# Optimization experiments

Measured on AMD Instinct MI355X. Metric: run time of the kernel, lower is better.

Reference implementation:

```python
import jax, jax.numpy as jnp
import numpy as np

N_NODES = 50000
N_EDGES = 1600000
D = 64


def setup_inputs() -> dict:
    key = jax.random.key(0)
    ks = jax.random.split(key, 7)
    scale = 1.0 / np.sqrt(2 * D)  # keep activations sane through relu stack
    x = jax.random.normal(ks[0], (N_NODES, D), dtype=jnp.float32)
    edge_index = jax.random.randint(ks[1], (2, N_EDGES), 0, N_NODES, dtype=jnp.int32)
    edge_weight = jax.random.uniform(ks[2], (N_EDGES,), dtype=jnp.float32)
    W1 = jax.random.normal(ks[3], (D, 2 * D), dtype=jnp.float32) * scale
    b1 = jax.random.normal(ks[4], (D,), dtype=jnp.float32) * 0.01
    W2 = jax.random.normal(ks[5], (D, 2 * D), dtype=jnp.float32) * scale
    b2 = jax.random.normal(ks[6], (D,), dtype=jnp.float32) * 0.01
    return {"x": x, "edge_index": edge_index, "edge_weight": edge_weight,
            "W1": W1, "b1": b1, "W2": W2, "b2": b2}


def _sage_conv(x, src, dst, edge_weight, W, b):
    # gather neighbor features, weight, scatter-mean onto src nodes
    m = x[dst] * edge_weight[:, None]                      # [E, d]
    agg_sum = jax.ops.segment_sum(m, src, num_segments=x.shape[0])
    cnt = jax.ops.segment_sum(jnp.ones_like(edge_weight), src,
                              num_segments=x.shape[0])
    agg = agg_sum / jnp.maximum(cnt, 1.0)[:, None]          # scatter 'mean'
    h = jnp.concatenate([x, agg], axis=1)                   # [N, 2d]
    return h @ W.T + b


def reference(x, edge_index, edge_weight, W1, b1, W2, b2):
    src, dst = edge_index[0], edge_index[1]
    h = jax.nn.relu(_sage_conv(x, src, dst, edge_weight, W1, b1))
    h = jax.nn.relu(_sage_conv(h, src, dst, edge_weight, W2, b2))
    return h
```

## Files before the change

### kernel.cpp

```cpp
#include <hip/hip_runtime.h>

#define NN 50000
#define NE 1600000
#define DD 64
#define NPB 196
#define HPB 98
#define NBKT 256
#define CHUNK 2500
#define NBLK 640
#define SLOT 24
#define SSTR 25
#define S1CAP 1024
#define SPCAP 512
#define ELLW 80

typedef __attribute__((ext_vector_type(8))) short bf16x8;
typedef __attribute__((ext_vector_type(4))) float f32x4;
typedef __attribute__((ext_vector_type(2))) float f32x2;

static __device__ __forceinline__ unsigned short f2bf(float f) {
    unsigned int u = __float_as_uint(f);
    unsigned int r = (u + 0x7FFFu + ((u >> 16) & 1u)) >> 16;
    return (unsigned short)r;
}
static __device__ __forceinline__ float bf2f(unsigned short h) {
    return __uint_as_float((unsigned int)h << 16);
}
static __device__ __forceinline__ unsigned int pk_fp8x4(float a, float b, float c, float d) {
    unsigned int p = __builtin_amdgcn_cvt_pk_fp8_f32(a, b, 0u, false);
    p = __builtin_amdgcn_cvt_pk_fp8_f32(c, d, p, true);
    return p;
}

__global__ __launch_bounds__(256) void prep_bin(
    const int* __restrict__ ei, const float* __restrict__ ew,
    int* __restrict__ gcur, int* __restrict__ gspillc,
    int2* __restrict__ buf1, int2* __restrict__ spill,
    const float* __restrict__ x, ushort* __restrict__ xb,
    unsigned int* __restrict__ xf8,
    const float* __restrict__ W1, const float* __restrict__ W2,
    ushort* __restrict__ W1b, ushort* __restrict__ W2b)
{
    __shared__ int2 slot[NBKT * SSTR];
    __shared__ int  lcnt[NBKT];
    __shared__ int  lbase[NBKT];
    int tid = threadIdx.x;
    int blk = blockIdx.x;

    if (blk >= NBLK) {
        int pb = blk - NBLK;
        if (pb < 3125) {
            int i = pb * 256 + tid;
            float4 v = ((const float4*)x)[i];
            ushort4 o;
            o.x = f2bf(v.x); o.y = f2bf(v.y); o.z = f2bf(v.z); o.w = f2bf(v.w);
            ((ushort4*)xb)[i] = o;
            xf8[i] = pk_fp8x4(v.x, v.y, v.z, v.w);
        } else {
            int i = (pb - 3125) * 256 + tid;
            const float* src = (i < 2048) ? W1 : W2;
            ushort* dst = (i < 2048) ? W1b : W2b;
            int j = i & 2047;
            float4 v = ((const float4*)src)[j];
            ushort4 o;
            o.x = f2bf(v.x); o.y = f2bf(v.y); o.z = f2bf(v.z); o.w = f2bf(v.w);
            ((ushort4*)dst)[j] = o;
        }
        return;
    }

    int shard = blk & 7;
    for (int b = tid; b < NBKT; b += 256) lcnt[b] = 0;
    __syncthreads();

    int g0 = blk * (CHUNK / 4);
    const int4*   s4 = (const int4*)ei;
    const int4*   d4 = ((const int4*)ei) + NE / 4;
    const float4* w4 = (const float4*)ew;
    for (int it = 0; it < 3; ++it) {
        int idx = it * 256 + tid;
        if (idx >= CHUNK / 4) break;
        int4 sv = s4[g0 + idx];
        int4 dv = d4[g0 + idx];
        float4 wv = w4[g0 + idx];
#pragma unroll
        for (int k = 0; k < 4; ++k) {
            int s = (k == 0) ? sv.x : (k == 1) ? sv.y : (k == 2) ? sv.z : sv.w;
            int d = (k == 0) ? dv.x : (k == 1) ? dv.y : (k == 2) ? dv.z : dv.w;
            float w = (k == 0) ? wv.x : (k == 1) ? wv.y : (k == 2) ? wv.z : wv.w;
            int bkt = s / NPB;
            int sloc = s - bkt * NPB;
            int2 rec = make_int2(d | ((int)f2bf(w) << 16), sloc);
            int pos = atomicAdd(&lcnt[bkt], 1);
            if (pos < SLOT) {
                slot[bkt * SSTR + pos] = rec;
            } else {
                int sp = atomicAdd(&gspillc[bkt], 1);
                if (sp < SPCAP) spill[bkt * SPCAP + sp] = rec;
            }
        }
    }
    __syncthreads();

    {
        int b = tid;
        int n = lcnt[b]; if (n > SLOT) n = SLOT;
        lcnt[b] = n;
        lbase[b] = (n > 0) ? atomicAdd(&gcur[b * 8 + shard], n) : 0;
    }
    __syncthreads();

    int wave = tid >> 6, lane = tid & 63;
    int grp = lane >> 4, l16 = lane & 15;
#pragma unroll 4
    for (int jj = 0; jj < 16; ++jj) {
        int b = wave * 64 + jj * 4 + grp;
        int n = lcnt[b];
        int base = lbase[b];
        int2* dst = &buf1[((size_t)b * 8 + shard) * S1CAP];
        if (l16 < n) {
            int2 rec = slot[b * SSTR + l16];
            int p = base + l16;
            if (p < S1CAP) dst[p] = rec;
            else { int sp = atomicAdd(&gspillc[b], 1);
                   if (sp < SPCAP) spill[b * SPCAP + sp] = rec; }
        }
        if (l16 + 16 < n) {
            int2 rec = slot[b * SSTR + l16 + 16];
            int p = base + l16 + 16;
            if (p < S1CAP) dst[p] = rec;
            else { int sp = atomicAdd(&gspillc[b], 1);
                   if (sp < SPCAP) spill[b * SPCAP + sp] = rec; }
        }
    }
}

__global__ __launch_bounds__(1024) void build_ell(
    const int* __restrict__ gcur, const int2* __restrict__ buf1,
    const int* __restrict__ gspillc, const int2* __restrict__ spill,
    unsigned int* __restrict__ csr, int* __restrict__ cnt)
{
    __shared__ int cur[HPB];
    __shared__ int cnts[9];
    int tid = threadIdx.x;
    int bkt  = blockIdx.x >> 1;
    int nlo  = (blockIdx.x & 1) * HPB;

    if (tid < HPB) cur[tid] = 0;
    if (tid >= 128 && tid < 137) {
        int sh = tid - 128;
        int n = (sh < 8) ? gcur[bkt * 8 + sh] : gspillc[bkt];
        int cap = (sh < 8) ? S1CAP : SPCAP;
        cnts[sh] = n < cap ? n : cap;
    }
    __syncthreads();

    {
        int sh = tid >> 7, lt = tid & 127;
        int n = cnts[sh];
        const int2* rp = buf1 + ((size_t)bkt * 8 + sh) * S1CAP;
        for (int i = lt; i < n; i += 128) {
            int2 r = rp[i];
            int node = r.y - nlo;
            if ((unsigned)node < HPB) {
                int pos = atomicAdd(&cur[node], 1);
                if (pos < ELLW)
                    csr[((size_t)(bkt * NPB + r.y)) * ELLW + pos] = (unsigned int)r.x;
            }
        }
    }
    {
        int n = cnts[8];
        const int2* rp = spill + (size_t)bkt * SPCAP;
        for (int i = tid; i < n; i += 1024) {
            int2 r = rp[i];
            int node = r.y - nlo;
            if ((unsigned)node < HPB) {
                int pos = atomicAdd(&cur[node], 1);
                if (pos < ELLW)
                    csr[((size_t)(bkt * NPB + r.y)) * ELLW + pos] = (unsigned int)r.x;
            }
        }
    }
    __syncthreads();

    if (tid < HPB) {
        int node = bkt * NPB + nlo + tid;
        if (node < NN) {
            int deg = cur[tid];
            cnt[node] = deg;
            int c = deg < ELLW ? deg : ELLW;
            int c16 = (c + 15) & ~15;
            for (int p = c; p < c16; ++p)
                csr[(size_t)node * ELLW + p] = 0u;
        }
    }
}

#define PROC16(r, s01, s23)                                                   \
    {                                                                         \
        unsigned int v0 = f8[(r.x & 0xFFFF) * 16 + l16];                      \
        unsigned int v1 = f8[(r.y & 0xFFFF) * 16 + l16];                      \
        unsigned int v2 = f8[(r.z & 0xFFFF) * 16 + l16];                      \
        unsigned int v3 = f8[(r.w & 0xFFFF) * 16 + l16];                      \
        float w0 = __uint_as_float(r.x & 0xFFFF0000u);                        \
        float w1 = __uint_as_float(r.y & 0xFFFF0000u);                        \
        float w2 = __uint_as_float(r.z & 0xFFFF0000u);                        \
        float w3 = __uint_as_float(r.w & 0xFFFF0000u);                        \
        f32x2 lo, hi, wp;                                                     \
        lo = __builtin_amdgcn_cvt_pk_f32_fp8(v0, false);                      \
        hi = __builtin_amdgcn_cvt_pk_f32_fp8(v0, true);                       \
        wp = (f32x2){w0, w0}; s01 += wp * lo; s23 += wp * hi;                 \
        lo = __builtin_amdgcn_cvt_pk_f32_fp8(v1, false);                      \
        hi = __builtin_amdgcn_cvt_pk_f32_fp8(v1, true);                       \
        wp = (f32x2){w1, w1}; s01 += wp * lo; s23 += wp * hi;                 \
        lo = __builtin_amdgcn_cvt_pk_f32_fp8(v2, false);                      \
        hi = __builtin_amdgcn_cvt_pk_f32_fp8(v2, true);                       \
        wp = (f32x2){w2, w2}; s01 += wp * lo; s23 += wp * hi;                 \
        lo = __builtin_amdgcn_cvt_pk_f32_fp8(v3, false);                      \
        hi = __builtin_amdgcn_cvt_pk_f32_fp8(v3, true);                       \
        wp = (f32x2){w3, w3}; s01 += wp * lo; s23 += wp * hi;                 \
    }

__global__ __launch_bounds__(512) void fused_layer(
    const ushort* __restrict__ Xb,
    const unsigned int* __restrict__ f8,
    const int* __restrict__ cnt, const unsigned int* __restrict__ csr,
    const ushort* __restrict__ Wb, const float* __restrict__ bias,
    float* __restrict__ out, ushort* __restrict__ outb,
    unsigned char* __restrict__ outf8)
{
    __shared__ ushort xL[16][72];
    __shared__ ushort aggL[16][72];
    int tid = threadIdx.x;
    int wave = tid >> 6, lane = tid & 63;
    int g = lane >> 4, l16 = lane & 15;
    int base = blockIdx.x * 16;
    int nodeA = base + wave;
    int nodeB = base + wave + 8;

    if (lane < 16) {
        *(ushort4*)&xL[wave][l16 * 4] =
            *(const ushort4*)&Xb[(size_t)nodeA * DD + l16 * 4];
        *(ushort4*)&xL[wave + 8][l16 * 4] =
            *(const ushort4*)&Xb[(size_t)nodeB * DD + l16 * 4];
    }

    int ndA = cnt[nodeA], ndB = cnt[nodeB];
    int nA = ndA < ELLW ? ndA : ELLW;
    int nB = ndB < ELLW ? ndB : ELLW;
    int nA16 = (nA + 15) & ~15;
    int nB16 = (nB + 15) & ~15;
    int imax = nA16 > nB16 ? nA16 : nB16;
    const unsigned int* __restrict__ rpA = csr + (size_t)nodeA * ELLW + g * 4;
    const unsigned int* __restrict__ rpB = csr + (size_t)nodeB * ELLW + g * 4;
    f32x2 sA01 = {0.f, 0.f}, sA23 = {0.f, 0.f};
    f32x2 sB01 = {0.f, 0.f}, sB23 = {0.f, 0.f};

    uint4 rA, rB;
    if (0 < nA16) rA = *(const uint4*)(rpA);
    if (0 < nB16) rB = *(const uint4*)(rpB);

    for (int i = 0; i < imax; i += 16) {
        uint4 rAn, rBn;
        bool doAn = (i + 16) < nA16, doBn = (i + 16) < nB16;
        if (doAn) rAn = *(const uint4*)(rpA + i + 16);
        if (doBn) rBn = *(const uint4*)(rpB + i + 16);
        bool doA = i < nA16, doB = i < nB16;
        if (doA) PROC16(rA, sA01, sA23);
        if (doB) PROC16(rB, sB01, sB23);
        rA = rAn; rB = rBn;
    }

    float aA0 = sA01.x, aA1 = sA01.y, aA2 = sA23.x, aA3 = sA23.y;
    float aB0 = sB01.x, aB1 = sB01.y, aB2 = sB23.x, aB3 = sB23.y;
    aA0 += __shfl_xor(aA0, 16); aA0 += __shfl_xor(aA0, 32);
    aA1 += __shfl_xor(aA1, 16); aA1 += __shfl_xor(aA1, 32);
    aA2 += __shfl_xor(aA2, 16); aA2 += __shfl_xor(aA2, 32);
    aA3 += __shfl_xor(aA3, 16); aA3 += __shfl_xor(aA3, 32);
    aB0 += __shfl_xor(aB0, 16); aB0 += __shfl_xor(aB0, 32);
    aB1 += __shfl_xor(aB1, 16); aB1 += __shfl_xor(aB1, 32);
    aB2 += __shfl_xor(aB2, 16); aB2 += __shfl_xor(aB2, 32);
    aB3 += __shfl_xor(aB3, 16); aB3 += __shfl_xor(aB3, 32);

    if (lane < 16) {
        float dmA = (float)(ndA > 1 ? ndA : 1);
        float dmB = (float)(ndB > 1 ? ndB : 1);
        ushort4 oA, oB;
        oA.x = f2bf(aA0 / dmA); oA.y = f2bf(aA1 / dmA);
        oA.z = f2bf(aA2 / dmA); oA.w = f2bf(aA3 / dmA);
        oB.x = f2bf(aB0 / dmB); oB.y = f2bf(aB1 / dmB);
        oB.z = f2bf(aB2 / dmB); oB.w = f2bf(aB3 / dmB);
        *(ushort4*)&aggL[wave][l16 * 4] = oA;
        *(ushort4*)&aggL[wave + 8][l16 * 4] = oB;
    }
    __syncthreads();

    if (wave < 4) {
        f32x4 acc = (f32x4){0.f, 0.f, 0.f, 0.f};
#pragma unroll
        for (int ki = 0; ki < 4; ++ki) {
            const ushort* ap = (ki < 2) ? &xL[l16][ki * 32 + g * 8]
                                        : &aggL[l16][(ki - 2) * 32 + g * 8];
            bf16x8 af = *(const bf16x8*)ap;
            bf16x8 bfrag = *(const bf16x8*)&Wb[(size_t)(wave * 16 + l16) * 128 + ki * 32 + g * 8];
            acc = __builtin_amdgcn_mfma_f32_16x16x32_bf16(af, bfrag, acc, 0, 0, 0);
        }
        int col = wave * 16 + l16;
        float bv = bias[col];
#pragma unroll
        for (int r = 0; r < 4; ++r) {
            int grow = base + g * 4 + r;
            float v = fmaxf(acc[r] + bv, 0.f);
            if (out)  out[(size_t)grow * DD + col] = v;
            if (outb) outb[(size_t)grow * DD + col] = f2bf(v);
            if (outf8) {
                unsigned int p = __builtin_amdgcn_cvt_pk_fp8_f32(v, v, 0u, false);
                outf8[(size_t)grow * DD + col] = (unsigned char)(p & 0xFFu);
            }
        }
    }
}

extern "C" void kernel_launch(void* const* d_in, const int* in_sizes, int n_in,
                              void* d_out, int out_size, void* d_ws, size_t ws_size,
                              hipStream_t stream)
{
    const float* x  = (const float*)d_in[0];
    const int*   ei = (const int*)d_in[1];
    const float* ew = (const float*)d_in[2];
    const float* W1 = (const float*)d_in[3];
    const float* b1 = (const float*)d_in[4];
    const float* W2 = (const float*)d_in[5];
    const float* b2 = (const float*)d_in[6];
    float* out = (float*)d_out;

    char* ws = (char*)d_ws;
    int*          gcur    = (int*)ws;
    int*          gspillc = (int*)(ws + 8192);
    int2*         buf1    = (int2*)(ws + 16384);
    int2*         spill   = (int2*)(ws + 16793600);
    unsigned int* csr     = (unsigned int*)(ws + 17842176);
    int*          cnt     = (int*)(ws + 33898496);
    ushort*       xb      = (ushort*)(ws + 34099200);
    ushort*       h1b     = (ushort*)(ws + 40499200);
    ushort*       W1b     = (ushort*)(ws + 46899200);
    ushort*       W2b     = (ushort*)(ws + 46915584);
    unsigned int* xf8     = (unsigned int*)(ws + 46931968);
    unsigned char* h1f8   = (unsigned char*)(ws + 50131968);

    hipMemsetAsync(gcur, 0, 9216, stream);

    prep_bin<<<NBLK + 3141, 256, 0, stream>>>(ei, ew, gcur, gspillc, buf1, spill,
                                              x, xb, xf8, W1, W2, W1b, W2b);
    build_ell<<<NBKT * 2, 1024, 0, stream>>>(gcur, buf1, gspillc, spill, csr, cnt);

    fused_layer<<<NN / 16, 512, 0, stream>>>(xb, xf8, cnt, csr, W1b, b1,
                                             nullptr, h1b, h1f8);
    fused_layer<<<NN / 16, 512, 0, stream>>>(h1b, (const unsigned int*)h1f8,
                                             cnt, csr, W2b, b2, out, nullptr, nullptr);
}
```

Measured before the change: 172.4 us.

## Merge all stages into one persistent kernel with software grid barriers

Replaces the four kernel launches (binning, ELL build, two fused SAGE layers) with a single persistent kernel of 512 blocks of 1024 threads. The stages are separated by atomic-counter grid barriers, and shared memory is reused through a union. This removes launch gaps and tail effects between stages. In exchange, the grid barriers add spin cost, occupancy during the layers is fixed, and correctness relies on all 512 blocks being co-resident.

```diff
diff --git a/kernel.cpp b/kernel.cpp
--- a/kernel.cpp
+++ b/kernel.cpp
@@ -6,13 +6,15 @@
 #define NPB 196
 #define HPB 98
 #define NBKT 256
-#define CHUNK 2500
-#define NBLK 640
+#define NCHUNK 640
+#define CG 625
 #define SLOT 24
 #define SSTR 25
 #define S1CAP 1024
 #define SPCAP 512
 #define ELLW 80
+#define GRID 512
+#define NTILE 1563
 
 typedef __attribute__((ext_vector_type(8))) short bf16x8;
 typedef __attribute__((ext_vector_type(4))) float f32x4;
@@ -23,178 +25,31 @@
     unsigned int r = (u + 0x7FFFu + ((u >> 16) & 1u)) >> 16;
     return (unsigned short)r;
 }
-static __device__ __forceinline__ float bf2f(unsigned short h) {
-    return __uint_as_float((unsigned int)h << 16);
-}
 static __device__ __forceinline__ unsigned int pk_fp8x4(float a, float b, float c, float d) {
     unsigned int p = __builtin_amdgcn_cvt_pk_fp8_f32(a, b, 0u, false);
     p = __builtin_amdgcn_cvt_pk_fp8_f32(c, d, p, true);
     return p;
 }
 
-__global__ __launch_bounds__(256) void prep_bin(
-    const int* __restrict__ ei, const float* __restrict__ ew,
-    int* __restrict__ gcur, int* __restrict__ gspillc,
-    int2* __restrict__ buf1, int2* __restrict__ spill,
-    const float* __restrict__ x, ushort* __restrict__ xb,
-    unsigned int* __restrict__ xf8,
-    const float* __restrict__ W1, const float* __restrict__ W2,
-    ushort* __restrict__ W1b, ushort* __restrict__ W2b)
-{
-    __shared__ int2 slot[NBKT * SSTR];
-    __shared__ int  lcnt[NBKT];
-    __shared__ int  lbase[NBKT];
-    int tid = threadIdx.x;
-    int blk = blockIdx.x;
-
-    if (blk >= NBLK) {
-        int pb = blk - NBLK;
-        if (pb < 3125) {
-            int i = pb * 256 + tid;
-            float4 v = ((const float4*)x)[i];
-            ushort4 o;
-            o.x = f2bf(v.x); o.y = f2bf(v.y); o.z = f2bf(v.z); o.w = f2bf(v.w);
-            ((ushort4*)xb)[i] = o;
-            xf8[i] = pk_fp8x4(v.x, v.y, v.z, v.w);
+static __device__ __forceinline__ void gridbar(int* bar) {
+    __syncthreads();
+    if (threadIdx.x == 0) {
+        int my = __hip_atomic_load(&bar[1], __ATOMIC_RELAXED, __HIP_MEMORY_SCOPE_AGENT);
+        __threadfence();
+        if (atomicAdd(&bar[0], 1) == GRID - 1) {
+            bar[0] = 0;
+            __threadfence();
+            __hip_atomic_store(&bar[1], my + 1, __ATOMIC_RELEASE, __HIP_MEMORY_SCOPE_AGENT);
         } else {
-            int i = (pb - 3125) * 256 + tid;
-            const float* src = (i < 2048) ? W1 : W2;
-            ushort* dst = (i < 2048) ? W1b : W2b;
-            int j = i & 2047;
-            float4 v = ((const float4*)src)[j];
-            ushort4 o;
-            o.x = f2bf(v.x); o.y = f2bf(v.y); o.z = f2bf(v.z); o.w = f2bf(v.w);
-            ((ushort4*)dst)[j] = o;
-        }
-        return;
-    }
-
-    int shard = blk & 7;
-    for (int b = tid; b < NBKT; b += 256) lcnt[b] = 0;
+            int t = 0;
+            while (__hip_atomic_load(&bar[1], __ATOMIC_ACQUIRE, __HIP_MEMORY_SCOPE_AGENT) == my) {
+                __builtin_amdgcn_s_sleep(4);
+                if (++t > (1 << 22)) break;
+            }
+        }
+        __threadfence();
+    }
     __syncthreads();
-
-    int g0 = blk * (CHUNK / 4);
-    const int4*   s4 = (const int4*)ei;
-    const int4*   d4 = ((const int4*)ei) + NE / 4;
-    const float4* w4 = (const float4*)ew;
-    for (int it = 0; it < 3; ++it) {
-        int idx = it * 256 + tid;
-        if (idx >= CHUNK / 4) break;
-        int4 sv = s4[g0 + idx];
-        int4 dv = d4[g0 + idx];
-        float4 wv = w4[g0 + idx];
-#pragma unroll
-        for (int k = 0; k < 4; ++k) {
-            int s = (k == 0) ? sv.x : (k == 1) ? sv.y : (k == 2) ? sv.z : sv.w;
-            int d = (k == 0) ? dv.x : (k == 1) ? dv.y : (k == 2) ? dv.z : dv.w;
-            float w = (k == 0) ? wv.x : (k == 1) ? wv.y : (k == 2) ? wv.z : wv.w;
-            int bkt = s / NPB;
-            int sloc = s - bkt * NPB;
-            int2 rec = make_int2(d | ((int)f2bf(w) << 16), sloc);
-            int pos = atomicAdd(&lcnt[bkt], 1);
-            if (pos < SLOT) {
-                slot[bkt * SSTR + pos] = rec;
-            } else {
-                int sp = atomicAdd(&gspillc[bkt], 1);
-                if (sp < SPCAP) spill[bkt * SPCAP + sp] = rec;
-            }
-        }
-    }
-    __syncthreads();
-
-    {
-        int b = tid;
-        int n = lcnt[b]; if (n > SLOT) n = SLOT;
-        lcnt[b] = n;
-        lbase[b] = (n > 0) ? atomicAdd(&gcur[b * 8 + shard], n) : 0;
-    }
-    __syncthreads();
-
-    int wave = tid >> 6, lane = tid & 63;
-    int grp = lane >> 4, l16 = lane & 15;
-#pragma unroll 4
-    for (int jj = 0; jj < 16; ++jj) {
-        int b = wave * 64 + jj * 4 + grp;
-        int n = lcnt[b];
-        int base = lbase[b];
-        int2* dst = &buf1[((size_t)b * 8 + shard) * S1CAP];
-        if (l16 < n) {
-            int2 rec = slot[b * SSTR + l16];
-            int p = base + l16;
-            if (p < S1CAP) dst[p] = rec;
-            else { int sp = atomicAdd(&gspillc[b], 1);
-                   if (sp < SPCAP) spill[b * SPCAP + sp] = rec; }
-        }
-        if (l16 + 16 < n) {
-            int2 rec = slot[b * SSTR + l16 + 16];
-            int p = base + l16 + 16;
-            if (p < S1CAP) dst[p] = rec;
-            else { int sp = atomicAdd(&gspillc[b], 1);
-                   if (sp < SPCAP) spill[b * SPCAP + sp] = rec; }
-        }
-    }
-}
-
-__global__ __launch_bounds__(1024) void build_ell(
-    const int* __restrict__ gcur, const int2* __restrict__ buf1,
-    const int* __restrict__ gspillc, const int2* __restrict__ spill,
-    unsigned int* __restrict__ csr, int* __restrict__ cnt)
-{
-    __shared__ int cur[HPB];
-    __shared__ int cnts[9];
-    int tid = threadIdx.x;
-    int bkt  = blockIdx.x >> 1;
-    int nlo  = (blockIdx.x & 1) * HPB;
-
-    if (tid < HPB) cur[tid] = 0;
-    if (tid >= 128 && tid < 137) {
-        int sh = tid - 128;
-        int n = (sh < 8) ? gcur[bkt * 8 + sh] : gspillc[bkt];
-        int cap = (sh < 8) ? S1CAP : SPCAP;
-        cnts[sh] = n < cap ? n : cap;
-    }
-    __syncthreads();
-
-    {
-        int sh = tid >> 7, lt = tid & 127;
-        int n = cnts[sh];
-        const int2* rp = buf1 + ((size_t)bkt * 8 + sh) * S1CAP;
-        for (int i = lt; i < n; i += 128) {
-            int2 r = rp[i];
-            int node = r.y - nlo;
-            if ((unsigned)node < HPB) {
-                int pos = atomicAdd(&cur[node], 1);
-                if (pos < ELLW)
-                    csr[((size_t)(bkt * NPB + r.y)) * ELLW + pos] = (unsigned int)r.x;
-            }
-        }
-    }
-    {
-        int n = cnts[8];
-        const int2* rp = spill + (size_t)bkt * SPCAP;
-        for (int i = tid; i < n; i += 1024) {
-            int2 r = rp[i];
-            int node = r.y - nlo;
-            if ((unsigned)node < HPB) {
-                int pos = atomicAdd(&cur[node], 1);
-                if (pos < ELLW)
-                    csr[((size_t)(bkt * NPB + r.y)) * ELLW + pos] = (unsigned int)r.x;
-            }
-        }
-    }
-    __syncthreads();
-
-    if (tid < HPB) {
-        int node = bkt * NPB + nlo + tid;
-        if (node < NN) {
-            int deg = cur[tid];
-            cnt[node] = deg;
-            int c = deg < ELLW ? deg : ELLW;
-            int c16 = (c + 15) & ~15;
-            for (int p = c; p < c16; ++p)
-                csr[(size_t)node * ELLW + p] = 0u;
-        }
-    }
 }
 
 #define PROC16(r, s01, s23)                                                   \
@@ -222,104 +77,285 @@
         wp = (f32x2){w3, w3}; s01 += wp * lo; s23 += wp * hi;                 \
     }
 
-__global__ __launch_bounds__(512) void fused_layer(
-    const ushort* __restrict__ Xb,
-    const unsigned int* __restrict__ f8,
+static __device__ void fused_phase(
+    const ushort* __restrict__ Xb, const unsigned int* __restrict__ f8,
     const int* __restrict__ cnt, const unsigned int* __restrict__ csr,
     const ushort* __restrict__ Wb, const float* __restrict__ bias,
     float* __restrict__ out, ushort* __restrict__ outb,
-    unsigned char* __restrict__ outf8)
+    unsigned char* __restrict__ outf8,
+    ushort (*xL)[72], ushort (*aggL)[72])
 {
-    __shared__ ushort xL[16][72];
-    __shared__ ushort aggL[16][72];
     int tid = threadIdx.x;
     int wave = tid >> 6, lane = tid & 63;
+    int sub = wave >> 3, w8 = wave & 7;
     int g = lane >> 4, l16 = lane & 15;
-    int base = blockIdx.x * 16;
-    int nodeA = base + wave;
-    int nodeB = base + wave + 8;
-
-    if (lane < 16) {
-        *(ushort4*)&xL[wave][l16 * 4] =
-            *(const ushort4*)&Xb[(size_t)nodeA * DD + l16 * 4];
-        *(ushort4*)&xL[wave + 8][l16 * 4] =
-            *(const ushort4*)&Xb[(size_t)nodeB * DD + l16 * 4];
-    }
-
-    int ndA = cnt[nodeA], ndB = cnt[nodeB];
-    int nA = ndA < ELLW ? ndA : ELLW;
-    int nB = ndB < ELLW ? ndB : ELLW;
-    int nA16 = (nA + 15) & ~15;
-    int nB16 = (nB + 15) & ~15;
-    int imax = nA16 > nB16 ? nA16 : nB16;
-    const unsigned int* __restrict__ rpA = csr + (size_t)nodeA * ELLW + g * 4;
-    const unsigned int* __restrict__ rpB = csr + (size_t)nodeB * ELLW + g * 4;
-    f32x2 sA01 = {0.f, 0.f}, sA23 = {0.f, 0.f};
-    f32x2 sB01 = {0.f, 0.f}, sB23 = {0.f, 0.f};
-
-    uint4 rA, rB;
-    if (0 < nA16) rA = *(const uint4*)(rpA);
-    if (0 < nB16) rB = *(const uint4*)(rpB);
-
-    for (int i = 0; i < imax; i += 16) {
-        uint4 rAn, rBn;
-        bool doAn = (i + 16) < nA16, doBn = (i + 16) < nB16;
-        if (doAn) rAn = *(const uint4*)(rpA + i + 16);
-        if (doBn) rBn = *(const uint4*)(rpB + i + 16);
-        bool doA = i < nA16, doB = i < nB16;
-        if (doA) PROC16(rA, sA01, sA23);
-        if (doB) PROC16(rB, sB01, sB23);
-        rA = rAn; rB = rBn;
-    }
-
-    float aA0 = sA01.x, aA1 = sA01.y, aA2 = sA23.x, aA3 = sA23.y;
-    float aB0 = sB01.x, aB1 = sB01.y, aB2 = sB23.x, aB3 = sB23.y;
-    aA0 += __shfl_xor(aA0, 16); aA0 += __shfl_xor(aA0, 32);
-    aA1 += __shfl_xor(aA1, 16); aA1 += __shfl_xor(aA1, 32);
-    aA2 += __shfl_xor(aA2, 16); aA2 += __shfl_xor(aA2, 32);
-    aA3 += __shfl_xor(aA3, 16); aA3 += __shfl_xor(aA3, 32);
-    aB0 += __shfl_xor(aB0, 16); aB0 += __shfl_xor(aB0, 32);
-    aB1 += __shfl_xor(aB1, 16); aB1 += __shfl_xor(aB1, 32);
-    aB2 += __shfl_xor(aB2, 16); aB2 += __shfl_xor(aB2, 32);
-    aB3 += __shfl_xor(aB3, 16); aB3 += __shfl_xor(aB3, 32);
-
-    if (lane < 16) {
-        float dmA = (float)(ndA > 1 ? ndA : 1);
-        float dmB = (float)(ndB > 1 ? ndB : 1);
-        ushort4 oA, oB;
-        oA.x = f2bf(aA0 / dmA); oA.y = f2bf(aA1 / dmA);
-        oA.z = f2bf(aA2 / dmA); oA.w = f2bf(aA3 / dmA);
-        oB.x = f2bf(aB0 / dmB); oB.y = f2bf(aB1 / dmB);
-        oB.z = f2bf(aB2 / dmB); oB.w = f2bf(aB3 / dmB);
-        *(ushort4*)&aggL[wave][l16 * 4] = oA;
-        *(ushort4*)&aggL[wave + 8][l16 * 4] = oB;
-    }
-    __syncthreads();
-
-    if (wave < 4) {
-        f32x4 acc = (f32x4){0.f, 0.f, 0.f, 0.f};
+
+    for (int t = blockIdx.x; t < NTILE; t += GRID) {
+        int base16 = t * 32 + sub * 16;
+        int nodeA = base16 + w8;
+        int nodeB = base16 + w8 + 8;
+        bool vA = nodeA < NN, vB = nodeB < NN;
+        int rowA = sub * 16 + w8, rowB = rowA + 8;
+
+        if (lane < 16) {
+            ushort4 z = make_ushort4(0, 0, 0, 0);
+            *(ushort4*)&xL[rowA][l16 * 4] = vA
+                ? *(const ushort4*)&Xb[(size_t)nodeA * DD + l16 * 4] : z;
+            *(ushort4*)&xL[rowB][l16 * 4] = vB
+                ? *(const ushort4*)&Xb[(size_t)nodeB * DD + l16 * 4] : z;
+        }
+
+        int ndA = vA ? cnt[nodeA] : 0;
+        int ndB = vB ? cnt[nodeB] : 0;
+        int nA = ndA < ELLW ? ndA : ELLW;
+        int nB = ndB < ELLW ? ndB : ELLW;
+        int nA16 = (nA + 15) & ~15;
+        int nB16 = (nB + 15) & ~15;
+        int imax = nA16 > nB16 ? nA16 : nB16;
+        const unsigned int* rpA = csr + (size_t)(vA ? nodeA : 0) * ELLW + g * 4;
+        const unsigned int* rpB = csr + (size_t)(vB ? nodeB : 0) * ELLW + g * 4;
+        f32x2 sA01 = {0.f, 0.f}, sA23 = {0.f, 0.f};
+        f32x2 sB01 = {0.f, 0.f}, sB23 = {0.f, 0.f};
+
+        uint4 rA, rB;
+        if (0 < nA16) rA = *(const uint4*)(rpA);
+        if (0 < nB16) rB = *(const uint4*)(rpB);
+
+        for (int i = 0; i < imax; i += 16) {
+            uint4 rAn, rBn;
+            bool doAn = (i + 16) < nA16, doBn = (i + 16) < nB16;
+            if (doAn) rAn = *(const uint4*)(rpA + i + 16);
+            if (doBn) rBn = *(const uint4*)(rpB + i + 16);
+            if (i < nA16) PROC16(rA, sA01, sA23);
+            if (i < nB16) PROC16(rB, sB01, sB23);
+            rA = rAn; rB = rBn;
+        }
+
+        float aA0 = sA01.x, aA1 = sA01.y, aA2 = sA23.x, aA3 = sA23.y;
+        float aB0 = sB01.x, aB1 = sB01.y, aB2 = sB23.x, aB3 = sB23.y;
+        aA0 += __shfl_xor(aA0, 16); aA0 += __shfl_xor(aA0, 32);
+        aA1 += __shfl_xor(aA1, 16); aA1 += __shfl_xor(aA1, 32);
+        aA2 += __shfl_xor(aA2, 16); aA2 += __shfl_xor(aA2, 32);
+        aA3 += __shfl_xor(aA3, 16); aA3 += __shfl_xor(aA3, 32);
+        aB0 += __shfl_xor(aB0, 16); aB0 += __shfl_xor(aB0, 32);
+        aB1 += __shfl_xor(aB1, 16); aB1 += __shfl_xor(aB1, 32);
+        aB2 += __shfl_xor(aB2, 16); aB2 += __shfl_xor(aB2, 32);
+        aB3 += __shfl_xor(aB3, 16); aB3 += __shfl_xor(aB3, 32);
+
+        if (lane < 16) {
+            float dmA = (float)(ndA > 1 ? ndA : 1);
+            float dmB = (float)(ndB > 1 ? ndB : 1);
+            ushort4 oA, oB;
+            oA.x = f2bf(aA0 / dmA); oA.y = f2bf(aA1 / dmA);
+            oA.z = f2bf(aA2 / dmA); oA.w = f2bf(aA3 / dmA);
+            oB.x = f2bf(aB0 / dmB); oB.y = f2bf(aB1 / dmB);
+            oB.z = f2bf(aB2 / dmB); oB.w = f2bf(aB3 / dmB);
+            *(ushort4*)&aggL[rowA][l16 * 4] = oA;
+            *(ushort4*)&aggL[rowB][l16 * 4] = oB;
+        }
+        __syncthreads();
+
+        if (w8 < 4) {
+            f32x4 acc = (f32x4){0.f, 0.f, 0.f, 0.f};
 #pragma unroll
-        for (int ki = 0; ki < 4; ++ki) {
-            const ushort* ap = (ki < 2) ? &xL[l16][ki * 32 + g * 8]
-                                        : &aggL[l16][(ki - 2) * 32 + g * 8];
-            bf16x8 af = *(const bf16x8*)ap;
-            bf16x8 bfrag = *(const bf16x8*)&Wb[(size_t)(wave * 16 + l16) * 128 + ki * 32 + g * 8];
-            acc = __builtin_amdgcn_mfma_f32_16x16x32_bf16(af, bfrag, acc, 0, 0, 0);
-        }
-        int col = wave * 16 + l16;
-        float bv = bias[col];
+            for (int ki = 0; ki < 4; ++ki) {
+                const ushort* ap = (ki < 2) ? &xL[sub * 16 + l16][ki * 32 + g * 8]
+                                            : &aggL[sub * 16 + l16][(ki - 2) * 32 + g * 8];
+                bf16x8 af = *(const bf16x8*)ap;
+                bf16x8 bfrag = *(const bf16x8*)&Wb[(size_t)(w8 * 16 + l16) * 128 + ki * 32 + g * 8];
+                acc = __builtin_amdgcn_mfma_f32_16x16x32_bf16(af, bfrag, acc, 0, 0, 0);
+            }
+            int col = w8 * 16 + l16;
+            float bv = bias[col];
 #pragma unroll
-        for (int r = 0; r < 4; ++r) {
-            int grow = base + g * 4 + r;
-            float v = fmaxf(acc[r] + bv, 0.f);
-            if (out)  out[(size_t)grow * DD + col] = v;
-            if (outb) outb[(size_t)grow * DD + col] = f2bf(v);
-            if (outf8) {
-                unsigned int p = __builtin_amdgcn_cvt_pk_fp8_f32(v, v, 0u, false);
-                outf8[(size_t)grow * DD + col] = (unsigned char)(p & 0xFFu);
-            }
-        }
-    }
+            for (int r = 0; r < 4; ++r) {
+                int grow = base16 + g * 4 + r;
+                if (grow < NN) {
+                    float v = fmaxf(acc[r] + bv, 0.f);
+                    if (out)  out[(size_t)grow * DD + col] = v;
+                    if (outb) outb[(size_t)grow * DD + col] = f2bf(v);
+                    if (outf8) {
+                        unsigned int p = __builtin_amdgcn_cvt_pk_fp8_f32(v, v, 0u, false);
+                        outf8[(size_t)grow * DD + col] = (unsigned char)(p & 0xFFu);
+                    }
+                }
+            }
+        }
+        __syncthreads();
+    }
+}
+
+__global__ __launch_bounds__(1024, 8) void mega(
+    const int* __restrict__ ei, const float* __restrict__ ew,
+    int* __restrict__ gcur, int* __restrict__ gspillc, int* bar,
+    int2* __restrict__ buf1, int2* __restrict__ spill,
+    unsigned int* __restrict__ csr, int* __restrict__ cnt,
+    const float* __restrict__ x, ushort* __restrict__ xb,
+    unsigned int* __restrict__ xf8,
+    const float* __restrict__ W1, const float* __restrict__ W2,
+    ushort* __restrict__ W1b, ushort* __restrict__ W2b,
+    const float* __restrict__ b1, const float* __restrict__ b2,
+    ushort* __restrict__ h1b, unsigned char* __restrict__ h1f8,
+    float* __restrict__ out)
+{
+    __shared__ union {
+        struct { int2 slot[NBKT * SSTR]; int lcnt[NBKT]; int lbase[NBKT]; } bin;
+        struct { int cur[HPB]; int cnts[9]; } bld;
+        struct { ushort xL[32][72]; ushort aggL[32][72]; } fl;
+    } sm;
+
+    int tid = threadIdx.x;
+    int wave = tid >> 6, lane = tid & 63;
+
+    {
+        const int4*   s4 = (const int4*)ei;
+        const int4*   d4 = ((const int4*)ei) + NE / 4;
+        const float4* w4 = (const float4*)ew;
+        for (int c = blockIdx.x; c < NCHUNK; c += GRID) {
+            if (tid < NBKT) sm.bin.lcnt[tid] = 0;
+            __syncthreads();
+            int shard = c & 7;
+            int g0 = c * CG;
+            if (tid < CG) {
+                int4 sv = s4[g0 + tid];
+                int4 dv = d4[g0 + tid];
+                float4 wv = w4[g0 + tid];
+#pragma unroll
+                for (int k = 0; k < 4; ++k) {
+                    int s = (k == 0) ? sv.x : (k == 1) ? sv.y : (k == 2) ? sv.z : sv.w;
+                    int d = (k == 0) ? dv.x : (k == 1) ? dv.y : (k == 2) ? dv.z : dv.w;
+                    float w = (k == 0) ? wv.x : (k == 1) ? wv.y : (k == 2) ? wv.z : wv.w;
+                    int bkt = s / NPB;
+                    int sloc = s - bkt * NPB;
+                    int2 rec = make_int2(d | ((int)f2bf(w) << 16), sloc);
+                    int pos = atomicAdd(&sm.bin.lcnt[bkt], 1);
+                    if (pos < SLOT) {
+                        sm.bin.slot[bkt * SSTR + pos] = rec;
+                    } else {
+                        int sp = atomicAdd(&gspillc[bkt], 1);
+                        if (sp < SPCAP) spill[bkt * SPCAP + sp] = rec;
+                    }
+                }
+            }
+            __syncthreads();
+            if (tid < NBKT) {
+                int b = tid;
+                int n = sm.bin.lcnt[b]; if (n > SLOT) n = SLOT;
+                sm.bin.lcnt[b] = n;
+                sm.bin.lbase[b] = (n > 0) ? atomicAdd(&gcur[b * 8 + shard], n) : 0;
+            }
+            __syncthreads();
+            int grp = lane >> 4, l16 = lane & 15;
+#pragma unroll 4
+            for (int jj = 0; jj < 4; ++jj) {
+                int b = wave * 16 + jj * 4 + grp;
+                int n = sm.bin.lcnt[b];
+                int base = sm.bin.lbase[b];
+                int2* dst = &buf1[((size_t)b * 8 + shard) * S1CAP];
+                if (l16 < n) {
+                    int2 rec = sm.bin.slot[b * SSTR + l16];
+                    int p = base + l16;
+                    if (p < S1CAP) dst[p] = rec;
+                    else { int sp = atomicAdd(&gspillc[b], 1);
+                           if (sp < SPCAP) spill[b * SPCAP + sp] = rec; }
+                }
+                if (l16 + 16 < n) {
+                    int2 rec = sm.bin.slot[b * SSTR + l16 + 16];
+                    int p = base + l16 + 16;
+                    if (p < S1CAP) dst[p] = rec;
+                    else { int sp = atomicAdd(&gspillc[b], 1);
+                           if (sp < SPCAP) spill[b * SPCAP + sp] = rec; }
+                }
+            }
+            __syncthreads();
+        }
+    }
+
+    for (int i = blockIdx.x * 1024 + tid; i < 804096; i += GRID * 1024) {
+        if (i < 800000) {
+            float4 v = ((const float4*)x)[i];
+            ushort4 o;
+            o.x = f2bf(v.x); o.y = f2bf(v.y); o.z = f2bf(v.z); o.w = f2bf(v.w);
+            ((ushort4*)xb)[i] = o;
+            xf8[i] = pk_fp8x4(v.x, v.y, v.z, v.w);
+        } else {
+            int j = i - 800000;
+            const float* src = (j < 2048) ? W1 : W2;
+            ushort* dst = (j < 2048) ? W1b : W2b;
+            int jj = j & 2047;
+            float4 v = ((const float4*)src)[jj];
+            ushort4 o;
+            o.x = f2bf(v.x); o.y = f2bf(v.y); o.z = f2bf(v.z); o.w = f2bf(v.w);
+            ((ushort4*)dst)[jj] = o;
+        }
+    }
+
+    gridbar(bar);
+
+    {
+        int bkt = blockIdx.x >> 1;
+        int nlo = (blockIdx.x & 1) * HPB;
+
+        if (tid < HPB) sm.bld.cur[tid] = 0;
+        if (tid >= 128 && tid < 137) {
+            int sh = tid - 128;
+            int n = (sh < 8) ? gcur[bkt * 8 + sh] : gspillc[bkt];
+            int cap = (sh < 8) ? S1CAP : SPCAP;
+            sm.bld.cnts[sh] = n < cap ? n : cap;
+        }
+        __syncthreads();
+
+        {
+            int sh = tid >> 7, lt = tid & 127;
+            int n = sm.bld.cnts[sh];
+            const int2* rp = buf1 + ((size_t)bkt * 8 + sh) * S1CAP;
+            for (int i = lt; i < n; i += 128) {
+                int2 r = rp[i];
+                int node = r.y - nlo;
+                if ((unsigned)node < HPB) {
+                    int pos = atomicAdd(&sm.bld.cur[node], 1);
+                    if (pos < ELLW)
+                        csr[((size_t)(bkt * NPB + r.y)) * ELLW + pos] = (unsigned int)r.x;
+                }
+            }
+        }
+        {
+            int n = sm.bld.cnts[8];
+            const int2* rp = spill + (size_t)bkt * SPCAP;
+            for (int i = tid; i < n; i += 1024) {
+                int2 r = rp[i];
+                int node = r.y - nlo;
+                if ((unsigned)node < HPB) {
+                    int pos = atomicAdd(&sm.bld.cur[node], 1);
+                    if (pos < ELLW)
+                        csr[((size_t)(bkt * NPB + r.y)) * ELLW + pos] = (unsigned int)r.x;
+                }
+            }
+        }
+        __syncthreads();
+
+        if (tid < HPB) {
+            int node = bkt * NPB + nlo + tid;
+            if (node < NN) {
+                int deg = sm.bld.cur[tid];
+                cnt[node] = deg;
+                int c = deg < ELLW ? deg : ELLW;
+                int c16 = (c + 15) & ~15;
+                for (int p = c; p < c16; ++p)
+                    csr[(size_t)node * ELLW + p] = 0u;
+            }
+        }
+    }
+
+    gridbar(bar);
+
+    fused_phase(xb, xf8, cnt, csr, W1b, b1,
+                nullptr, h1b, h1f8, sm.fl.xL, sm.fl.aggL);
+
+    gridbar(bar);
+
+    fused_phase(h1b, (const unsigned int*)h1f8, cnt, csr, W2b, b2,
+                out, nullptr, nullptr, sm.fl.xL, sm.fl.aggL);
 }
 
 extern "C" void kernel_launch(void* const* d_in, const int* in_sizes, int n_in,
@@ -338,6 +374,7 @@
     char* ws = (char*)d_ws;
     int*          gcur    = (int*)ws;
     int*          gspillc = (int*)(ws + 8192);
+    int*          bar     = (int*)(ws + 9216);
     int2*         buf1    = (int2*)(ws + 16384);
     int2*         spill   = (int2*)(ws + 16793600);
     unsigned int* csr     = (unsigned int*)(ws + 17842176);
@@ -349,14 +386,9 @@
     unsigned int* xf8     = (unsigned int*)(ws + 46931968);
     unsigned char* h1f8   = (unsigned char*)(ws + 50131968);
 
-    hipMemsetAsync(gcur, 0, 9216, stream);
-
-    prep_bin<<<NBLK + 3141, 256, 0, stream>>>(ei, ew, gcur, gspillc, buf1, spill,
-                                              x, xb, xf8, W1, W2, W1b, W2b);
-    build_ell<<<NBKT * 2, 1024, 0, stream>>>(gcur, buf1, gspillc, spill, csr, cnt);
-
-    fused_layer<<<NN / 16, 512, 0, stream>>>(xb, xf8, cnt, csr, W1b, b1,
-                                             nullptr, h1b, h1f8);
-    fused_layer<<<NN / 16, 512, 0, stream>>>(h1b, (const unsigned int*)h1f8,
-                                             cnt, csr, W2b, b2, out, nullptr, nullptr);
-}
+    hipMemsetAsync(gcur, 0, 9232, stream);
+
+    mega<<<GRID, 1024, 0, stream>>>(ei, ew, gcur, gspillc, bar, buf1, spill,
+                                    csr, cnt, x, xb, xf8, W1, W2, W1b, W2b,
+                                    b1, b2, h1b, h1f8, out);
+}
```

New measurement: 486.2 us. 182% more time.
